# Kernel optimization log

Hardware: AMD Instinct MI355X
Metric: run time of the kernel (lower is better)

The kernel has to match this reference:

```python
import jax, jax.numpy as jnp
import numpy as np

P = 16        # patch size
WIN = 64      # attention window size
NH = 12       # num heads


def _layernorm(x, g, b, eps=1e-5):
    m = x.mean(-1, keepdims=True)
    v = ((x - m) ** 2).mean(-1, keepdims=True)
    return (x - m) * jax.lax.rsqrt(v + eps) * g + b


def _sinusoidal_pe(n, d):
    pos = jnp.arange(n, dtype=jnp.float32)[:, None]
    i = jnp.arange(d // 2, dtype=jnp.float32)[None, :]
    ang = pos / jnp.power(10000.0, (2.0 * i) / d)
    pe = jnp.zeros((n, d), jnp.float32)
    pe = pe.at[:, 0::2].set(jnp.sin(ang)).at[:, 1::2].set(jnp.cos(ang))
    return pe


def setup_inputs() -> dict:
    key = jax.random.key(0)
    ks = jax.random.split(key, 8)
    B, C, H, W, D, F = 16, 3, 512, 512, 768, 3072
    s = lambda k, shape: (jax.random.normal(k, shape, jnp.float32) * 0.02)
    return {
        "input": jax.random.normal(ks[0], (B, C, H, W), jnp.float32),
        "patch_w": s(ks[1], (D, C, P, P)),
        "patch_b": jnp.zeros((D,), jnp.float32),
        "ln_g": jnp.ones((D,), jnp.float32),
        "ln_b": jnp.zeros((D,), jnp.float32),
        "qkv_w": s(ks[2], (D, 3 * D)),
        "qkv_b": jnp.zeros((3 * D,), jnp.float32),
        "proj_w": s(ks[3], (D, D)),
        "proj_b": jnp.zeros((D,), jnp.float32),
        "ff1_w": s(ks[4], (D, F)),
        "ff1_b": jnp.zeros((F,), jnp.float32),
        "ff2_w": s(ks[5], (F, D)),
        "ff2_b": jnp.zeros((D,), jnp.float32),
    }


def reference(input, patch_w, patch_b, ln_g, ln_b, qkv_w, qkv_b,
              proj_w, proj_b, ff1_w, ff1_b, ff2_w, ff2_b):
    B, C, H, W = input.shape
    D = patch_w.shape[0]
    dh = D // NH
    # --- patch embedding (conv k=stride=P as einsum) + norm ---
    xp = input.reshape(B, C, H // P, P, W // P, P)
    x = jnp.einsum('bchpwq,dcpq->bhwd', xp, patch_w) + patch_b  # [B,32,32,D]
    x = x.reshape(B, -1, D)                                      # [B,N,D]
    x = _layernorm(x, ln_g, ln_b)
    N = x.shape[1]
    # --- static sinusoidal position embedding ---
    x = x + _sinusoidal_pe(N, D)

    def ff(y):  # shared feedforward (dropout=eval/off)
        return jax.nn.gelu(y @ ff1_w + ff1_b) @ ff2_w + ff2_b

    def sparse_attn(y):  # windowed block-sparse attention, window=64
        nW = N // WIN
        qkv = (y @ qkv_w + qkv_b).reshape(B, nW, WIN, 3, NH, dh)
        q, k, v = qkv[:, :, :, 0], qkv[:, :, :, 1], qkv[:, :, :, 2]
        scores = jnp.einsum('bwqhd,bwkhd->bwhqk', q, k) * (dh ** -0.5)
        a = jax.nn.softmax(scores, axis=-1)
        o = jnp.einsum('bwhqk,bwkhd->bwqhd', a, v).reshape(B, N, D)
        return o @ proj_w + proj_b

    identity = x
    x = ff(x)
    x = sparse_attn(x)
    x = x + identity
    identity = x
    x = ff(x)
    x = x + identity
    return x
```

## Files before the change

kernel.cpp:

```cpp
#include <hip/hip_runtime.h>

typedef unsigned int uint;
typedef short bf16x8 __attribute__((ext_vector_type(8)));
typedef float f32x4 __attribute__((ext_vector_type(4)));

__device__ __forceinline__ unsigned short f2b(float f) {
    uint u = __builtin_bit_cast(uint, f);
    u += 0x7fffu + ((u >> 16) & 1u);
    return (unsigned short)(u >> 16);
}
__device__ __forceinline__ float b2f(unsigned short h) {
    uint u = ((uint)h) << 16;
    return __builtin_bit_cast(float, u);
}

__device__ __forceinline__ float fast_gelu(float v) {
    float s  = v * v;
    float t2 = __builtin_fmaf(0.044715f * s, v, v);
    float e  = __expf(-1.5957691216f * t2);
    return v * __builtin_amdgcn_rcpf(1.0f + e);
}

__device__ __forceinline__ void gl_lds16(const unsigned short* g, unsigned short* l) {
    __builtin_amdgcn_global_load_lds(
        reinterpret_cast<const __attribute__((address_space(1))) unsigned int*>(
            reinterpret_cast<uintptr_t>(g)),
        reinterpret_cast<__attribute__((address_space(3))) unsigned int*>(
            reinterpret_cast<uintptr_t>(l)),
        16, 0, 0);
}

__global__ __launch_bounds__(256) void convert_bf16_kernel(const float* __restrict__ src,
                                                           unsigned short* __restrict__ dst, int n) {
    int idx = blockIdx.x * 256 + threadIdx.x;
    if (idx < n) dst[idx] = f2b(src[idx]);
}

__global__ __launch_bounds__(256) void transpose_to_bf16_kernel(const float* __restrict__ src,
                                                                unsigned short* __restrict__ dst,
                                                                int K, int N) {
    long long idx = (long long)blockIdx.x * 256 + threadIdx.x;
    if (idx >= (long long)K * N) return;
    int k = (int)(idx / N);
    int n = (int)(idx % N);
    dst[(long long)n * K + k] = f2b(src[idx]);
}

__global__ __launch_bounds__(256) void im2col_kernel(const float* __restrict__ in,
                                                     unsigned short* __restrict__ out) {
    long long idx = (long long)blockIdx.x * 256 + threadIdx.x;
    int k = (int)(idx % 768);
    int n = (int)(idx / 768);
    int b = n >> 10, t = n & 1023;
    int hp = t >> 5, wp = t & 31;
    int c = k >> 8, rm = k & 255;
    int p = rm >> 4, q = rm & 15;
    long long src = (((long long)(b * 3 + c) * 512) + hp * 16 + p) * 512 + wp * 16 + q;
    out[idx] = f2b(in[src]);
}

__global__ __launch_bounds__(256) void ln_pe_kernel(const float* __restrict__ xe,
                                                    const float* __restrict__ g,
                                                    const float* __restrict__ bb,
                                                    unsigned short* __restrict__ xb) {
    int row = blockIdx.x;
    int pos = row & 1023;
    const float* xr = xe + (long long)row * 768;
    float v0 = xr[threadIdx.x];
    float v1 = xr[threadIdx.x + 256];
    float v2 = xr[threadIdx.x + 512];
    float s = v0 + v1 + v2;
    float sq = v0 * v0 + v1 * v1 + v2 * v2;
    for (int o = 32; o > 0; o >>= 1) {
        s  += __shfl_down(s, o, 64);
        sq += __shfl_down(sq, o, 64);
    }
    __shared__ float ps[4], pq[4];
    int w = threadIdx.x >> 6, lane = threadIdx.x & 63;
    if (lane == 0) { ps[w] = s; pq[w] = sq; }
    __syncthreads();
    float ts = ps[0] + ps[1] + ps[2] + ps[3];
    float tq = pq[0] + pq[1] + pq[2] + pq[3];
    float mean = ts * (1.0f / 768.0f);
    float var  = tq * (1.0f / 768.0f) - mean * mean;
    float inv  = rsqrtf(var + 1e-5f);
    #pragma unroll
    for (int dd = 0; dd < 3; dd++) {
        int d = threadIdx.x + dd * 256;
        float val = (dd == 0) ? v0 : (dd == 1) ? v1 : v2;
        float y = (val - mean) * inv * g[d] + bb[d];
        float freq = __expf(-(float)(d & ~1) * (9.210340371976184f / 768.0f));
        float ang = (float)pos * freq;
        y += (d & 1) ? cosf(ang) : sinf(ang);
        xb[(long long)row * 768 + d] = f2b(y);
    }
}

__global__ __launch_bounds__(256) void gemm128_kernel(const unsigned short* __restrict__ A,
                                                      const unsigned short* __restrict__ BT,
                                                      const float* __restrict__ bias,
                                                      const unsigned short* __restrict__ residB,
                                                      float* __restrict__ outF,
                                                      unsigned short* __restrict__ outB,
                                                      int M, int N, int K, int ldb,
                                                      int epi, int accumF) {
    __shared__ unsigned short As[128 * 32];
    __shared__ unsigned short Bs[128 * 32];

    const int nX = N >> 7;
    int id = blockIdx.x;
    int xcd = id & 7;
    int sq_ = id >> 3;
    int bx = sq_ % nX;
    int by = (sq_ / nX) * 8 + xcd;

    const int tid = threadIdx.x;
    const int m0 = by * 128, n0 = bx * 128;
    const int w = tid >> 6, lane = tid & 63;
    const int wm = (w >> 1) * 64, wn = (w & 1) * 64;
    const int quad = lane >> 4, l15 = lane & 15;

    const int srow = tid >> 2;
    const int scol = (tid & 3) * 8;
    const unsigned short* Ag0 = A  + (long long)(m0 + srow) * K + scol;
    const unsigned short* Ag1 = Ag0 + (long long)64 * K;
    const unsigned short* Bg0 = BT + (long long)(n0 + srow) * ldb + scol;
    const unsigned short* Bg1 = Bg0 + (long long)64 * ldb;
    unsigned short* Ad0 = As + srow * 32 + scol;
    unsigned short* Ad1 = Ad0 + 64 * 32;
    unsigned short* Bd0 = Bs + srow * 32 + scol;
    unsigned short* Bd1 = Bd0 + 64 * 32;

    f32x4 acc[4][4] = {};

    for (int k0 = 0; k0 < K; k0 += 32) {
        __syncthreads();
        gl_lds16(Ag0 + k0, Ad0);
        gl_lds16(Ag1 + k0, Ad1);
        gl_lds16(Bg0 + k0, Bd0);
        gl_lds16(Bg1 + k0, Bd1);
        __syncthreads();

        bf16x8 af[4], bfr[4];
        #pragma unroll
        for (int i = 0; i < 4; i++)
            af[i] = *(const bf16x8*)(As + (wm + i * 16 + l15) * 32 + quad * 8);
        #pragma unroll
        for (int j = 0; j < 4; j++)
            bfr[j] = *(const bf16x8*)(Bs + (wn + j * 16 + l15) * 32 + quad * 8);
        #pragma unroll
        for (int i = 0; i < 4; i++)
            #pragma unroll
            for (int j = 0; j < 4; j++)
                acc[i][j] = __builtin_amdgcn_mfma_f32_16x16x32_bf16(af[i], bfr[j], acc[i][j], 0, 0, 0);
    }

    const int r0 = quad * 4;
    #pragma unroll
    for (int i = 0; i < 4; i++) {
        #pragma unroll
        for (int j = 0; j < 4; j++) {
            int gn = n0 + wn + j * 16 + l15;
            float bv = bias ? bias[gn] : 0.0f;
            #pragma unroll
            for (int r = 0; r < 4; r++) {
                int gm = m0 + wm + i * 16 + r0 + r;
                float v = acc[i][j][r] + bv;
                if (epi == 1) v = fast_gelu(v);
                long long off = (long long)gm * N + gn;
                if (accumF) v += outF[off];
                if (residB) v += b2f(residB[off]);
                if (outF) outF[off] = v;
                if (outB) outB[off] = f2b(v);
            }
        }
    }
}

__global__ __launch_bounds__(256) void attn_kernel(const unsigned short* __restrict__ qkv,
                                                   unsigned short* __restrict__ o) {
    __shared__ float qs[64 * 65], ks[64 * 65], vs[64 * 65];
    __shared__ float pmax[4 * 64], psum[4 * 64];
    int blk = blockIdx.x;
    int h = blk % 12;
    int bw = blk / 12;
    int wi = bw % 16, b = bw / 16;
    int rowBase = b * 1024 + wi * 64;
    int tid = threadIdx.x;

    int lr = tid >> 2, c0 = (tid & 3) * 16;
    const unsigned short* src = qkv + (long long)(rowBase + lr) * 2304 + h * 64 + c0;
    #pragma unroll
    for (int j = 0; j < 16; j++) {
        qs[lr * 65 + c0 + j] = b2f(src[j]);
        ks[lr * 65 + c0 + j] = b2f(src[768 + j]);
        vs[lr * 65 + c0 + j] = b2f(src[1536 + j]);
    }
    __syncthreads();

    int r = tid & 63, cg = tid >> 6;
    float svals[16] = {};
    for (int kk = 0; kk < 64; kk++) {
        float qv = qs[r * 65 + kk];
        #pragma unroll
        for (int j = 0; j < 16; j++)
            svals[j] += qv * ks[(cg * 16 + j) * 65 + kk];
    }
    float smax = -1e30f;
    #pragma unroll
    for (int j = 0; j < 16; j++) {
        svals[j] *= 0.125f;
        smax = fmaxf(smax, svals[j]);
    }
    pmax[cg * 64 + r] = smax;
    __syncthreads();
    float m = fmaxf(fmaxf(pmax[r], pmax[64 + r]), fmaxf(pmax[128 + r], pmax[192 + r]));
    float lsum = 0.0f;
    #pragma unroll
    for (int j = 0; j < 16; j++) {
        float e = __expf(svals[j] - m);
        qs[r * 65 + cg * 16 + j] = e;
        lsum += e;
    }
    psum[cg * 64 + r] = lsum;
    __syncthreads();
    float inv = __builtin_amdgcn_rcpf(psum[r] + psum[64 + r] + psum[128 + r] + psum[192 + r]);

    float oacc[16] = {};
    for (int c = 0; c < 64; c++) {
        float pv = qs[r * 65 + c];
        #pragma unroll
        for (int j = 0; j < 16; j++)
            oacc[j] += pv * vs[c * 65 + cg * 16 + j];
    }
    unsigned short* dst = o + (long long)(rowBase + r) * 768 + h * 64 + cg * 16;
    #pragma unroll
    for (int j = 0; j < 16; j++) dst[j] = f2b(oacc[j] * inv);
}

extern "C" void kernel_launch(void* const* d_in, const int* in_sizes, int n_in,
                              void* d_out, int out_size, void* d_ws, size_t ws_size,
                              hipStream_t stream) {
    const float* input   = (const float*)d_in[0];
    const float* patch_w = (const float*)d_in[1];
    const float* patch_b = (const float*)d_in[2];
    const float* ln_g    = (const float*)d_in[3];
    const float* ln_b    = (const float*)d_in[4];
    const float* qkv_w   = (const float*)d_in[5];
    const float* qkv_b   = (const float*)d_in[6];
    const float* proj_w  = (const float*)d_in[7];
    const float* proj_b  = (const float*)d_in[8];
    const float* ff1_w   = (const float*)d_in[9];
    const float* ff1_b   = (const float*)d_in[10];
    const float* ff2_w   = (const float*)d_in[11];
    const float* ff2_b   = (const float*)d_in[12];
    float* out = (float*)d_out;

    const int MN = 16384;
    const int D = 768, F = 3072, TD = 2304;
    const int NY = MN / 128;

    unsigned short* wPatch = (unsigned short*)d_ws;
    unsigned short* wQkvT  = wPatch + 589824;
    unsigned short* wProjT = wQkvT + 1769472;
    unsigned short* wFf1T  = wProjT + 589824;
    unsigned short* wFf2T  = wFf1T + 2359296;
    unsigned short* bigBuf = wFf2T + 2359296;
    unsigned short* xid    = bigBuf + 50331648;
    unsigned short* t0     = xid + 12582912;

    convert_bf16_kernel<<<(589824 + 255) / 256, 256, 0, stream>>>(patch_w, wPatch, 589824);
    transpose_to_bf16_kernel<<<(1769472 + 255) / 256, 256, 0, stream>>>(qkv_w, wQkvT, D, TD);
    transpose_to_bf16_kernel<<<(589824 + 255) / 256, 256, 0, stream>>>(proj_w, wProjT, D, D);
    transpose_to_bf16_kernel<<<(2359296 + 255) / 256, 256, 0, stream>>>(ff1_w, wFf1T, D, F);
    transpose_to_bf16_kernel<<<(2359296 + 255) / 256, 256, 0, stream>>>(ff2_w, wFf2T, F, D);

    im2col_kernel<<<(MN * 768) / 256, 256, 0, stream>>>(input, bigBuf);

    gemm128_kernel<<<(D / 128) * NY, 256, 0, stream>>>(bigBuf, wPatch, patch_b, nullptr,
                                                       out, nullptr, MN, D, 768, 768, 0, 0);
    ln_pe_kernel<<<MN, 256, 0, stream>>>(out, ln_g, ln_b, xid);

    gemm128_kernel<<<(F / 128) * NY, 256, 0, stream>>>(xid, wFf1T, ff1_b, nullptr,
                                                       nullptr, bigBuf, MN, F, 768, 768, 1, 0);
    gemm128_kernel<<<(D / 128) * NY, 256, 0, stream>>>(bigBuf, wFf2T, ff2_b, nullptr,
                                                       nullptr, t0, MN, D, F, F, 0, 0);
    gemm128_kernel<<<(TD / 128) * NY, 256, 0, stream>>>(t0, wQkvT, qkv_b, nullptr,
                                                        nullptr, bigBuf, MN, TD, 768, 768, 0, 0);
    attn_kernel<<<16 * 16 * 12, 256, 0, stream>>>(bigBuf, t0);

    gemm128_kernel<<<(D / 128) * NY, 256, 0, stream>>>(t0, wProjT, proj_b, xid,
                                                       nullptr, xid, MN, D, 768, 768, 0, 0);

    gemm128_kernel<<<(F / 128) * NY, 256, 0, stream>>>(xid, wFf1T, ff1_b, nullptr,
                                                       nullptr, bigBuf, MN, F, 768, 768, 1, 0);
    gemm128_kernel<<<(D / 128) * NY, 256, 0, stream>>>(bigBuf, wFf2T, ff2_b, xid,
                                                       out, nullptr, MN, D, F, F, 0, 0);
}
```

Measured before the change: 964.7 us.

## Double GEMM K-tile to 64 and XOR-swizzle LDS layout

Raises the K step of the 128x128 bf16 MFMA GEMM from 32 to 64, which halves the number of barrier pairs per K sweep and issues eight async global-to-LDS loads per thread per step instead of four. Each row's 16-byte column chunks are XOR-permuted by the row index on the global side, and the fragment reads apply the same XOR, so the wider 128-byte LDS rows avoid bank conflicts. LDS use per block doubles, which may lower occupancy. K must now be a multiple of 64.

Result: faster. 863.2 us (-10.5%).

```diff
diff --git a/kernel.cpp b/kernel.cpp
--- a/kernel.cpp
+++ b/kernel.cpp
@@ -104,8 +104,8 @@
                                                       unsigned short* __restrict__ outB,
                                                       int M, int N, int K, int ldb,
                                                       int epi, int accumF) {
-    __shared__ unsigned short As[128 * 32];
-    __shared__ unsigned short Bs[128 * 32];
+    __shared__ unsigned short As[128 * 64];
+    __shared__ unsigned short Bs[128 * 64];
 
     const int nX = N >> 7;
     int id = blockIdx.x;
@@ -120,39 +120,57 @@
     const int wm = (w >> 1) * 64, wn = (w & 1) * 64;
     const int quad = lane >> 4, l15 = lane & 15;
 
-    const int srow = tid >> 2;
-    const int scol = (tid & 3) * 8;
-    const unsigned short* Ag0 = A  + (long long)(m0 + srow) * K + scol;
-    const unsigned short* Ag1 = Ag0 + (long long)64 * K;
-    const unsigned short* Bg0 = BT + (long long)(n0 + srow) * ldb + scol;
-    const unsigned short* Bg1 = Bg0 + (long long)64 * ldb;
-    unsigned short* Ad0 = As + srow * 32 + scol;
-    unsigned short* Ad1 = Ad0 + 64 * 32;
-    unsigned short* Bd0 = Bs + srow * 32 + scol;
-    unsigned short* Bd1 = Bd0 + 64 * 32;
+    const int srow = tid >> 3;
+    const int sc8  = tid & 7;
+    const int gc8  = sc8 ^ (srow & 7);
+    const unsigned short* Ag0 = A  + (long long)(m0 + srow) * K + gc8 * 8;
+    const unsigned short* Ag1 = Ag0 + (long long)32 * K;
+    const unsigned short* Ag2 = Ag0 + (long long)64 * K;
+    const unsigned short* Ag3 = Ag0 + (long long)96 * K;
+    const unsigned short* Bg0 = BT + (long long)(n0 + srow) * ldb + gc8 * 8;
+    const unsigned short* Bg1 = Bg0 + (long long)32 * ldb;
+    const unsigned short* Bg2 = Bg0 + (long long)64 * ldb;
+    const unsigned short* Bg3 = Bg0 + (long long)96 * ldb;
+    unsigned short* Ad0 = As + srow * 64 + sc8 * 8;
+    unsigned short* Ad1 = Ad0 + 32 * 64;
+    unsigned short* Ad2 = Ad0 + 64 * 64;
+    unsigned short* Ad3 = Ad0 + 96 * 64;
+    unsigned short* Bd0 = Bs + srow * 64 + sc8 * 8;
+    unsigned short* Bd1 = Bd0 + 32 * 64;
+    unsigned short* Bd2 = Bd0 + 64 * 64;
+    unsigned short* Bd3 = Bd0 + 96 * 64;
 
     f32x4 acc[4][4] = {};
-
-    for (int k0 = 0; k0 < K; k0 += 32) {
+    const int swz = l15 & 7;
+
+    for (int k0 = 0; k0 < K; k0 += 64) {
         __syncthreads();
         gl_lds16(Ag0 + k0, Ad0);
         gl_lds16(Ag1 + k0, Ad1);
+        gl_lds16(Ag2 + k0, Ad2);
+        gl_lds16(Ag3 + k0, Ad3);
         gl_lds16(Bg0 + k0, Bd0);
         gl_lds16(Bg1 + k0, Bd1);
+        gl_lds16(Bg2 + k0, Bd2);
+        gl_lds16(Bg3 + k0, Bd3);
         __syncthreads();
 
-        bf16x8 af[4], bfr[4];
         #pragma unroll
-        for (int i = 0; i < 4; i++)
-            af[i] = *(const bf16x8*)(As + (wm + i * 16 + l15) * 32 + quad * 8);
-        #pragma unroll
-        for (int j = 0; j < 4; j++)
-            bfr[j] = *(const bf16x8*)(Bs + (wn + j * 16 + l15) * 32 + quad * 8);
-        #pragma unroll
-        for (int i = 0; i < 4; i++)
+        for (int h = 0; h < 2; h++) {
+            const int c8 = h * 4 + quad;
+            bf16x8 af[4], bfr[4];
+            #pragma unroll
+            for (int i = 0; i < 4; i++)
+                af[i] = *(const bf16x8*)(As + (wm + i * 16 + l15) * 64 + ((c8 ^ swz) * 8));
             #pragma unroll
             for (int j = 0; j < 4; j++)
-                acc[i][j] = __builtin_amdgcn_mfma_f32_16x16x32_bf16(af[i], bfr[j], acc[i][j], 0, 0, 0);
+                bfr[j] = *(const bf16x8*)(Bs + (wn + j * 16 + l15) * 64 + ((c8 ^ swz) * 8));
+            #pragma unroll
+            for (int i = 0; i < 4; i++)
+                #pragma unroll
+                for (int j = 0; j < 4; j++)
+                    acc[i][j] = __builtin_amdgcn_mfma_f32_16x16x32_bf16(af[i], bfr[j], acc[i][j], 0, 0, 0);
+        }
     }
 
     const int r0 = quad * 4;
```

## Double-buffer GEMM LDS tiles with BK=64 and XOR-swizzled layout

Applied to the files above, without the earlier changes.

The bf16 GEMM main loop now uses two LDS buffers with a K-tile of 64 instead of one buffer with a K-tile of 32. Global-to-LDS loads for the next tile are issued before computing on the current one, so only one barrier is needed per iteration. Column chunks are XOR-swizzled by row to avoid LDS bank conflicts on the fragment reads. In exchange, LDS use per block grows to 64KB, which may limit how many blocks fit on a CU.

After: 956.5 us. Within noise of the previous version (-0.8%).

```diff
diff --git a/kernel.cpp b/kernel.cpp
--- a/kernel.cpp
+++ b/kernel.cpp
@@ -104,8 +104,8 @@
                                                       unsigned short* __restrict__ outB,
                                                       int M, int N, int K, int ldb,
                                                       int epi, int accumF) {
-    __shared__ unsigned short As[128 * 32];
-    __shared__ unsigned short Bs[128 * 32];
+    __shared__ unsigned short As[2][128 * 64];
+    __shared__ unsigned short Bs[2][128 * 64];
 
     const int nX = N >> 7;
     int id = blockIdx.x;
@@ -120,39 +120,68 @@
     const int wm = (w >> 1) * 64, wn = (w & 1) * 64;
     const int quad = lane >> 4, l15 = lane & 15;
 
-    const int srow = tid >> 2;
-    const int scol = (tid & 3) * 8;
-    const unsigned short* Ag0 = A  + (long long)(m0 + srow) * K + scol;
-    const unsigned short* Ag1 = Ag0 + (long long)64 * K;
-    const unsigned short* Bg0 = BT + (long long)(n0 + srow) * ldb + scol;
-    const unsigned short* Bg1 = Bg0 + (long long)64 * ldb;
-    unsigned short* Ad0 = As + srow * 32 + scol;
-    unsigned short* Ad1 = Ad0 + 64 * 32;
-    unsigned short* Bd0 = Bs + srow * 32 + scol;
-    unsigned short* Bd1 = Bd0 + 64 * 32;
-
+    const int srow = tid >> 3;
+    const int sc8  = tid & 7;
+    const int gc8  = sc8 ^ (srow & 7);
+    const unsigned short* Ag = A  + (long long)(m0 + srow) * K + gc8 * 8;
+    const unsigned short* Bg = BT + (long long)(n0 + srow) * ldb + gc8 * 8;
+    const long long aStep = (long long)32 * K;
+    const long long bStep = (long long)32 * ldb;
+    const int ldsOff = srow * 64 + sc8 * 8;
+
+    const int nIter = K >> 6;
     f32x4 acc[4][4] = {};
-
-    for (int k0 = 0; k0 < K; k0 += 32) {
+    const int swz = l15 & 7;
+
+    {
+        unsigned short* Ad = &As[0][0] + ldsOff;
+        unsigned short* Bd = &Bs[0][0] + ldsOff;
+        gl_lds16(Ag,             Ad);
+        gl_lds16(Ag + aStep,     Ad + 32 * 64);
+        gl_lds16(Ag + 2 * aStep, Ad + 64 * 64);
+        gl_lds16(Ag + 3 * aStep, Ad + 96 * 64);
+        gl_lds16(Bg,             Bd);
+        gl_lds16(Bg + bStep,     Bd + 32 * 64);
+        gl_lds16(Bg + 2 * bStep, Bd + 64 * 64);
+        gl_lds16(Bg + 3 * bStep, Bd + 96 * 64);
+    }
+
+    for (int it = 0; it < nIter; ++it) {
+        const int cur = it & 1;
         __syncthreads();
-        gl_lds16(Ag0 + k0, Ad0);
-        gl_lds16(Ag1 + k0, Ad1);
-        gl_lds16(Bg0 + k0, Bd0);
-        gl_lds16(Bg1 + k0, Bd1);
-        __syncthreads();
-
-        bf16x8 af[4], bfr[4];
+
+        if (it + 1 < nIter) {
+            const int k0 = (it + 1) << 6;
+            unsigned short* Ad = &As[cur ^ 1][0] + ldsOff;
+            unsigned short* Bd = &Bs[cur ^ 1][0] + ldsOff;
+            gl_lds16(Ag + k0,             Ad);
+            gl_lds16(Ag + k0 + aStep,     Ad + 32 * 64);
+            gl_lds16(Ag + k0 + 2 * aStep, Ad + 64 * 64);
+            gl_lds16(Ag + k0 + 3 * aStep, Ad + 96 * 64);
+            gl_lds16(Bg + k0,             Bd);
+            gl_lds16(Bg + k0 + bStep,     Bd + 32 * 64);
+            gl_lds16(Bg + k0 + 2 * bStep, Bd + 64 * 64);
+            gl_lds16(Bg + k0 + 3 * bStep, Bd + 96 * 64);
+        }
+
+        const unsigned short* Ab = &As[cur][0];
+        const unsigned short* Bb = &Bs[cur][0];
         #pragma unroll
-        for (int i = 0; i < 4; i++)
-            af[i] = *(const bf16x8*)(As + (wm + i * 16 + l15) * 32 + quad * 8);
-        #pragma unroll
-        for (int j = 0; j < 4; j++)
-            bfr[j] = *(const bf16x8*)(Bs + (wn + j * 16 + l15) * 32 + quad * 8);
-        #pragma unroll
-        for (int i = 0; i < 4; i++)
+        for (int h = 0; h < 2; h++) {
+            const int c8 = h * 4 + quad;
+            bf16x8 af[4], bfr[4];
+            #pragma unroll
+            for (int i = 0; i < 4; i++)
+                af[i] = *(const bf16x8*)(Ab + (wm + i * 16 + l15) * 64 + ((c8 ^ swz) * 8));
             #pragma unroll
             for (int j = 0; j < 4; j++)
-                acc[i][j] = __builtin_amdgcn_mfma_f32_16x16x32_bf16(af[i], bfr[j], acc[i][j], 0, 0, 0);
+                bfr[j] = *(const bf16x8*)(Bb + (wn + j * 16 + l15) * 64 + ((c8 ^ swz) * 8));
+            #pragma unroll
+            for (int i = 0; i < 4; i++)
+                #pragma unroll
+                for (int j = 0; j < 4; j++)
+                    acc[i][j] = __builtin_amdgcn_mfma_f32_16x16x32_bf16(af[i], bfr[j], acc[i][j], 0, 0, 0);
+        }
     }
 
     const int r0 = quad * 4;
```

## Add producer wave with double-buffered BK=64 LDS and XOR swizzle to GEMM

Applied to the files above, without the earlier changes.

The GEMM now launches 320 threads. A fifth wave only issues global-to-LDS loads into a double-buffered 128x64 tile for A and B, so fetching the next K-slice overlaps the four compute waves' MFMA work on the current one. The K step doubles to 64, which halves the number of barriers, and LDS columns are XOR-swizzled by row to reduce bank conflicts on fragment reads. The cost is 64KB of LDS per block, which limits occupancy, and one wave alone has to sustain all the load traffic. Correctness also depends on the barrier fence waiting for the asynchronous LDS loads to finish.

Result: slower. 1.084 ms (+12.4%).

```diff
diff --git a/kernel.cpp b/kernel.cpp
--- a/kernel.cpp
+++ b/kernel.cpp
@@ -96,7 +96,7 @@
     }
 }
 
-__global__ __launch_bounds__(256) void gemm128_kernel(const unsigned short* __restrict__ A,
+__global__ __launch_bounds__(320) void gemm128_kernel(const unsigned short* __restrict__ A,
                                                       const unsigned short* __restrict__ BT,
                                                       const float* __restrict__ bias,
                                                       const unsigned short* __restrict__ residB,
@@ -104,8 +104,8 @@
                                                       unsigned short* __restrict__ outB,
                                                       int M, int N, int K, int ldb,
                                                       int epi, int accumF) {
-    __shared__ unsigned short As[128 * 32];
-    __shared__ unsigned short Bs[128 * 32];
+    __shared__ unsigned short As[2][128 * 64];
+    __shared__ unsigned short Bs[2][128 * 64];
 
     const int nX = N >> 7;
     int id = blockIdx.x;
@@ -116,43 +116,66 @@
 
     const int tid = threadIdx.x;
     const int m0 = by * 128, n0 = bx * 128;
-    const int w = tid >> 6, lane = tid & 63;
-    const int wm = (w >> 1) * 64, wn = (w & 1) * 64;
+    const int wv = tid >> 6, lane = tid & 63;
+    const int nIter = K >> 6;
+
+    if (wv == 4) {
+        const int srow8 = lane >> 3;
+        const int sc8   = lane & 7;
+        const int gc8   = sc8 ^ srow8;
+        const unsigned short* Ab = A  + (long long)(m0 + srow8) * K   + gc8 * 8;
+        const unsigned short* Bb = BT + (long long)(n0 + srow8) * ldb + gc8 * 8;
+        const int ldsOff = srow8 * 64 + sc8 * 8;
+        const long long a8 = (long long)8 * K;
+        const long long b8 = (long long)8 * ldb;
+
+        #pragma unroll
+        for (int i = 0; i < 16; i++) {
+            gl_lds16(Ab + i * a8, &As[0][0] + ldsOff + i * 8 * 64);
+            gl_lds16(Bb + i * b8, &Bs[0][0] + ldsOff + i * 8 * 64);
+        }
+        for (int it = 0; it < nIter; ++it) {
+            __syncthreads();
+            if (it + 1 < nIter) {
+                const long long k0 = (long long)(it + 1) << 6;
+                unsigned short* Ad = &As[(it + 1) & 1][0] + ldsOff;
+                unsigned short* Bd = &Bs[(it + 1) & 1][0] + ldsOff;
+                #pragma unroll
+                for (int i = 0; i < 16; i++) {
+                    gl_lds16(Ab + k0 + i * a8, Ad + i * 8 * 64);
+                    gl_lds16(Bb + k0 + i * b8, Bd + i * 8 * 64);
+                }
+            }
+        }
+        return;
+    }
+
+    const int wm = (wv >> 1) * 64, wn = (wv & 1) * 64;
     const int quad = lane >> 4, l15 = lane & 15;
-
-    const int srow = tid >> 2;
-    const int scol = (tid & 3) * 8;
-    const unsigned short* Ag0 = A  + (long long)(m0 + srow) * K + scol;
-    const unsigned short* Ag1 = Ag0 + (long long)64 * K;
-    const unsigned short* Bg0 = BT + (long long)(n0 + srow) * ldb + scol;
-    const unsigned short* Bg1 = Bg0 + (long long)64 * ldb;
-    unsigned short* Ad0 = As + srow * 32 + scol;
-    unsigned short* Ad1 = Ad0 + 64 * 32;
-    unsigned short* Bd0 = Bs + srow * 32 + scol;
-    unsigned short* Bd1 = Bd0 + 64 * 32;
+    const int swz = l15 & 7;
 
     f32x4 acc[4][4] = {};
 
-    for (int k0 = 0; k0 < K; k0 += 32) {
+    for (int it = 0; it < nIter; ++it) {
         __syncthreads();
-        gl_lds16(Ag0 + k0, Ad0);
-        gl_lds16(Ag1 + k0, Ad1);
-        gl_lds16(Bg0 + k0, Bd0);
-        gl_lds16(Bg1 + k0, Bd1);
-        __syncthreads();
-
-        bf16x8 af[4], bfr[4];
-        #pragma unroll
-        for (int i = 0; i < 4; i++)
-            af[i] = *(const bf16x8*)(As + (wm + i * 16 + l15) * 32 + quad * 8);
-        #pragma unroll
-        for (int j = 0; j < 4; j++)
-            bfr[j] = *(const bf16x8*)(Bs + (wn + j * 16 + l15) * 32 + quad * 8);
-        #pragma unroll
-        for (int i = 0; i < 4; i++)
+        const unsigned short* Ab = &As[it & 1][0];
+        const unsigned short* Bb = &Bs[it & 1][0];
+        #pragma unroll
+        for (int h = 0; h < 2; h++) {
+            const int c8 = h * 4 + quad;
+            bf16x8 af[4], bfr[4];
+            #pragma unroll
+            for (int i = 0; i < 4; i++)
+                af[i] = *(const bf16x8*)(Ab + (wm + i * 16 + l15) * 64 + ((c8 ^ swz) * 8));
             #pragma unroll
             for (int j = 0; j < 4; j++)
-                acc[i][j] = __builtin_amdgcn_mfma_f32_16x16x32_bf16(af[i], bfr[j], acc[i][j], 0, 0, 0);
+                bfr[j] = *(const bf16x8*)(Bb + (wn + j * 16 + l15) * 64 + ((c8 ^ swz) * 8));
+            #pragma unroll
+            for (int i = 0; i < 4; i++)
+                #pragma unroll
+                for (int j = 0; j < 4; j++)
+                    acc[i][j] = __builtin_amdgcn_mfma_f32_16x16x32_bf16(af[i], bfr[j], acc[i][j], 0, 0, 0);
+        }
     }
 
     const int r0 = quad * 4;
@@ -277,23 +300,23 @@
 
     im2col_kernel<<<(MN * 768) / 256, 256, 0, stream>>>(input, bigBuf);
 
-    gemm128_kernel<<<(D / 128) * NY, 256, 0, stream>>>(bigBuf, wPatch, patch_b, nullptr,
+    gemm128_kernel<<<(D / 128) * NY, 320, 0, stream>>>(bigBuf, wPatch, patch_b, nullptr,
                                                        out, nullptr, MN, D, 768, 768, 0, 0);
     ln_pe_kernel<<<MN, 256, 0, stream>>>(out, ln_g, ln_b, xid);
 
-    gemm128_kernel<<<(F / 128) * NY, 256, 0, stream>>>(xid, wFf1T, ff1_b, nullptr,
+    gemm128_kernel<<<(F / 128) * NY, 320, 0, stream>>>(xid, wFf1T, ff1_b, nullptr,
                                                        nullptr, bigBuf, MN, F, 768, 768, 1, 0);
-    gemm128_kernel<<<(D / 128) * NY, 256, 0, stream>>>(bigBuf, wFf2T, ff2_b, nullptr,
+    gemm128_kernel<<<(D / 128) * NY, 320, 0, stream>>>(bigBuf, wFf2T, ff2_b, nullptr,
                                                        nullptr, t0, MN, D, F, F, 0, 0);
-    gemm128_kernel<<<(TD / 128) * NY, 256, 0, stream>>>(t0, wQkvT, qkv_b, nullptr,
+    gemm128_kernel<<<(TD / 128) * NY, 320, 0, stream>>>(t0, wQkvT, qkv_b, nullptr,
                                                         nullptr, bigBuf, MN, TD, 768, 768, 0, 0);
     attn_kernel<<<16 * 16 * 12, 256, 0, stream>>>(bigBuf, t0);
 
-    gemm128_kernel<<<(D / 128) * NY, 256, 0, stream>>>(t0, wProjT, proj_b, xid,
+    gemm128_kernel<<<(D / 128) * NY, 320, 0, stream>>>(t0, wProjT, proj_b, xid,
                                                        nullptr, xid, MN, D, 768, 768, 0, 0);
 
-    gemm128_kernel<<<(F / 128) * NY, 256, 0, stream>>>(xid, wFf1T, ff1_b, nullptr,
+    gemm128_kernel<<<(F / 128) * NY, 320, 0, stream>>>(xid, wFf1T, ff1_b, nullptr,
                                                        nullptr, bigBuf, MN, F, 768, 768, 1, 0);
-    gemm128_kernel<<<(D / 128) * NY, 256, 0, stream>>>(bigBuf, wFf2T, ff2_b, xid,
+    gemm128_kernel<<<(D / 128) * NY, 320, 0, stream>>>(bigBuf, wFf2T, ff2_b, xid,
                                                        out, nullptr, MN, D, F, F, 0, 0);
 }
```
